# Performance work log

Measured on AMD Instinct MI355X. Metric: run time of the kernel, lower is better.

Reference implementation:

```python
import jax, jax.numpy as jnp
import numpy as np

B, T, C = 2, 2048, 1024
N_HEAD = 16
HEAD_DIM = C // N_HEAD
N_WORLDS = 4


def setup_inputs() -> dict:
    key = jax.random.key(0)
    kx, kq, kk, kv, kp, ka = jax.random.split(key, 6)
    scale = 0.02
    x = jax.random.normal(kx, (B, T, C), dtype=jnp.float32)
    Wq = jax.random.normal(kq, (C, C), dtype=jnp.float32) * scale
    Wk = jax.random.normal(kk, (C, C), dtype=jnp.float32) * scale
    Wv = jax.random.normal(kv, (C, C), dtype=jnp.float32) * scale
    Wproj = jax.random.normal(kp, (C, C), dtype=jnp.float32) * scale
    acc = jax.random.randint(ka, (N_WORLDS, N_WORLDS), 0, 2, dtype=jnp.int32)
    # ensure every world accesses itself so no softmax row is fully masked
    acc = acc.at[jnp.arange(N_WORLDS), jnp.arange(N_WORLDS)].set(1)
    return {"x": x, "Wq": Wq, "Wk": Wk, "Wv": Wv, "Wproj": Wproj,
            "accessibility": acc}


def reference(x, Wq, Wk, Wv, Wproj, accessibility):
    Bd, Td, Cd = x.shape
    # torch Linear: y = x @ W.T  -> project then split heads
    q = (x @ Wq.T).reshape(Bd, Td, N_HEAD, HEAD_DIM).transpose(0, 2, 1, 3)
    k = (x @ Wk.T).reshape(Bd, Td, N_HEAD, HEAD_DIM).transpose(0, 2, 1, 3)
    v = (x @ Wv.T).reshape(Bd, Td, N_HEAD, HEAD_DIM).transpose(0, 2, 1, 3)

    scores = jnp.einsum('bhqd,bhkd->bhqk', q, k) / jnp.sqrt(
        jnp.asarray(HEAD_DIM, dtype=x.dtype))

    # Kripke modal mask: token t lives in world t % n_worlds (necessity: \u25a1)
    world = jnp.arange(Td) % accessibility.shape[0]
    modal_mask = accessibility[world][:, world]          # (T, T) 0/1
    scores = jnp.where(modal_mask[None, None] == 0, -jnp.inf, scores)

    attn = jax.nn.softmax(scores, axis=-1)
    out = jnp.einsum('bhqk,bhkd->bhqd', attn, v)
    out = out.transpose(0, 2, 1, 3).reshape(Bd, Td, Cd)
    return out @ Wproj.T
```

## Files before the change

### kernel.cpp

```cpp
#include <hip/hip_runtime.h>
#include <hip/hip_bf16.h>
#include <stdint.h>


typedef __attribute__((ext_vector_type(8))) __bf16   bf16x8;
typedef __attribute__((ext_vector_type(4))) float    f32x4;
typedef __attribute__((ext_vector_type(8))) ushort   ushort8;

__device__ __forceinline__ ushort f2bf(float x) {
    uint32_t u = __float_as_uint(x);
    return (ushort)((u + 0x7fffu + ((u >> 16) & 1u)) >> 16);
}
__device__ __forceinline__ float sentinel(float v, float s) {
    return (fabsf(v) < 1e30f) ? v : s;
}
__device__ __forceinline__ f32x4 mfma16(bf16x8 a, bf16x8 b, f32x4 c) {
    return __builtin_amdgcn_mfma_f32_16x16x32_bf16(a, b, c, 0, 0, 0);
}
__device__ __forceinline__ ushort2 pk2(float a, float b) {
    __hip_bfloat162 h = __float22bfloat162_rn(make_float2(a, b));
    union { __hip_bfloat162 h; ushort2 u; } c; c.h = h; return c.u;
}
__device__ __forceinline__ ushort4 cvt4(float4 v) {
    ushort2 lo = pk2(v.x, v.y), hi = pk2(v.z, v.w);
    ushort4 r; r.x = lo.x; r.y = lo.y; r.z = hi.x; r.w = hi.y; return r;
}
__device__ __forceinline__ ushort4 cvt4s(float4 v, float s) {
    ushort2 lo = pk2(v.x * s, v.y * s), hi = pk2(v.z * s, v.w * s);
    ushort4 r; r.x = lo.x; r.y = lo.y; r.z = hi.x; r.w = hi.y; return r;
}
__device__ __forceinline__ float fexp2(float x) {
#if __has_builtin(__builtin_amdgcn_exp2f)
    return __builtin_amdgcn_exp2f(x);
#else
    return exp2f(x);
#endif
}
__device__ __forceinline__ void gld16(const ushort* g, ushort* l) {
    auto* g1 = reinterpret_cast<const __attribute__((address_space(1))) uint32_t*>(
        reinterpret_cast<uintptr_t>(g));
    auto* l3 = reinterpret_cast<__attribute__((address_space(3))) uint32_t*>(
        reinterpret_cast<uintptr_t>(l));
    __builtin_amdgcn_global_load_lds(g1, l3, 16, 0, 0);
}

__device__ __forceinline__ int swz(int row, int ch) {
    return row * 64 + ((ch ^ (row & 7)) * 8);
}

#define QSCALE 0.1803368801111244f

__global__ __launch_bounds__(256) void cvt_prepass(
        const float* __restrict__ x,  const float* __restrict__ Wq,
        const float* __restrict__ Wk, const float* __restrict__ Wv,
        const float* __restrict__ Wp,
        ushort* __restrict__ xb,  ushort* __restrict__ wqb,
        ushort* __restrict__ wkb, ushort* __restrict__ wvb,
        ushort* __restrict__ wpb)
{
    int gid = blockIdx.x;
    const float* src; ushort* dst; float sc = 1.0f; int boff;
    if (gid < 4096)      { src = x;  dst = xb;  boff = gid; }
    else if (gid < 5120) { src = Wq; dst = wqb; boff = gid - 4096; sc = QSCALE; }
    else if (gid < 6144) { src = Wk; dst = wkb; boff = gid - 5120; }
    else if (gid < 7168) { src = Wv; dst = wvb; boff = gid - 6144; }
    else                 { src = Wp; dst = wpb; boff = gid - 7168; }
    size_t idx = (size_t)boff * 1024 + threadIdx.x * 4;
    float4 v = *(const float4*)&src[idx];
    *(ushort4*)&dst[idx] = cvt4s(v, sc);
}

__global__ __launch_bounds__(256) void gemm_qkv_b(
        const ushort* __restrict__ xb,
        const ushort* __restrict__ wqb, const ushort* __restrict__ wkb,
        const ushort* __restrict__ wvb,
        ushort* __restrict__ Cq, ushort* __restrict__ Ck,
        ushort* __restrict__ Cv)
{
    __shared__ ushort As[128 * 64];
    __shared__ ushort Bs[128 * 64];

    const int sel = blockIdx.x >> 3;
    const ushort* __restrict__ Bw = sel == 0 ? wqb : (sel == 1 ? wkb : wvb);
    ushort* __restrict__ C        = sel == 0 ? Cq : (sel == 1 ? Ck : Cv);

    const int tid  = threadIdx.x;
    const int lane = tid & 63;
    const int wave = tid >> 6;
    const int quad = lane >> 4;
    const int l15  = lane & 15;
    const int bm = blockIdx.y * 128;
    const int bn = (blockIdx.x & 7) * 128;
    const int wm = (wave & 1) * 64, wn = (wave >> 1) * 64;

    f32x4 acc[4][4] = {};

    for (int k0 = 0; k0 < 1024; k0 += 64) {
        __syncthreads();
        #pragma unroll
        for (int j = 0; j < 4; ++j) {
            int cb = j * 256 + wave * 64;
            int ci = cb + lane;
            int r  = ci >> 3;
            int qc = (ci & 7) ^ (r & 7);
            gld16(&xb[(size_t)(bm + r) * 1024 + k0 + qc * 8], &As[cb * 8]);
            gld16(&Bw[(size_t)(bn + r) * 1024 + k0 + qc * 8], &Bs[cb * 8]);
        }
        __syncthreads();

        bf16x8 af[2][4], bfr[2][4];
        #pragma unroll
        for (int f = 0; f < 2; ++f)
            #pragma unroll
            for (int i = 0; i < 4; ++i) {
                int ch = f * 4 + quad;
                af[f][i]  = *(const bf16x8*)&As[swz(wm + i * 16 + l15, ch)];
                bfr[f][i] = *(const bf16x8*)&Bs[swz(wn + i * 16 + l15, ch)];
            }
        #pragma unroll
        for (int f = 0; f < 2; ++f)
            #pragma unroll
            for (int i = 0; i < 4; ++i)
                #pragma unroll
                for (int t = 0; t < 4; ++t)
                    acc[i][t] = mfma16(af[f][i], bfr[f][t], acc[i][t]);
    }

    if (sel < 2) {
        #pragma unroll
        for (int i = 0; i < 4; ++i)
            #pragma unroll
            for (int t = 0; t < 4; ++t)
                #pragma unroll
                for (int r = 0; r < 4; ++r) {
                    int m = bm + wm + i * 16 + quad * 4 + r;
                    int n = bn + wn + t * 16 + l15;
                    int b = m >> 11, ts = m & 2047, hh = n >> 6, d = n & 63;
                    C[((size_t)((b << 4) | hh) * 2048 + ts) * 64 + d] =
                        f2bf(sentinel(acc[i][t][r], 1e8f));
                }
    } else {
        #pragma unroll
        for (int i = 0; i < 4; ++i)
            #pragma unroll
            for (int t = 0; t < 4; ++t) {
                int m0 = bm + wm + i * 16 + quad * 4;
                int n  = bn + wn + t * 16 + l15;
                int b = m0 >> 11, ts = m0 & 2047, hh = n >> 6, d = n & 63;
                ushort4 hv;
                hv.x = f2bf(sentinel(acc[i][t][0], 1e8f));
                hv.y = f2bf(sentinel(acc[i][t][1], 1e8f));
                hv.z = f2bf(sentinel(acc[i][t][2], 1e8f));
                hv.w = f2bf(sentinel(acc[i][t][3], 1e8f));
                *(ushort4*)&C[((size_t)((b << 4) | hh) * 64 + d) * 2048 + ts] = hv;
            }
    }
}

__global__ __launch_bounds__(256) void gemm_proj_b(
        const ushort* __restrict__ O, const ushort* __restrict__ wpb,
        float* __restrict__ out)
{
    __shared__ ushort As[128 * 64];
    __shared__ ushort Bs[64 * 64];

    const int tid  = threadIdx.x;
    const int lane = tid & 63;
    const int wave = tid >> 6;
    const int quad = lane >> 4;
    const int l15  = lane & 15;
    const int bm = blockIdx.y * 128, bn = blockIdx.x * 64;
    const int wm = (wave & 1) * 64,  wn = (wave >> 1) * 32;

    f32x4 acc[4][2] = {};

    for (int k0 = 0; k0 < 1024; k0 += 64) {
        __syncthreads();
        int h = k0 >> 6;
        #pragma unroll
        for (int j = 0; j < 4; ++j) {
            int cb = j * 256 + wave * 64;
            int ci = cb + lane;
            int r  = ci >> 3;
            int qc = (ci & 7) ^ (r & 7);
            int m = bm + r;
            int b = m >> 11, ts = m & 2047;
            gld16(&O[((((size_t)(b * 16 + h)) * 2048 + ts) << 6) + qc * 8],
                  &As[cb * 8]);
        }
        #pragma unroll
        for (int j = 0; j < 2; ++j) {
            int cb = j * 256 + wave * 64;
            int ci = cb + lane;
            int r  = ci >> 3;
            int qc = (ci & 7) ^ (r & 7);
            gld16(&wpb[(size_t)(bn + r) * 1024 + k0 + qc * 8], &Bs[cb * 8]);
        }
        __syncthreads();

        bf16x8 af[2][4], bfr[2][2];
        #pragma unroll
        for (int f = 0; f < 2; ++f) {
            int ch = f * 4 + quad;
            #pragma unroll
            for (int i = 0; i < 4; ++i)
                af[f][i] = *(const bf16x8*)&As[swz(wm + i * 16 + l15, ch)];
            #pragma unroll
            for (int t = 0; t < 2; ++t)
                bfr[f][t] = *(const bf16x8*)&Bs[swz(wn + t * 16 + l15, ch)];
        }
        #pragma unroll
        for (int f = 0; f < 2; ++f)
            #pragma unroll
            for (int i = 0; i < 4; ++i)
                #pragma unroll
                for (int t = 0; t < 2; ++t)
                    acc[i][t] = mfma16(af[f][i], bfr[f][t], acc[i][t]);
    }

    #pragma unroll
    for (int i = 0; i < 4; ++i)
        #pragma unroll
        for (int t = 0; t < 2; ++t)
            #pragma unroll
            for (int r = 0; r < 4; ++r) {
                int m = bm + wm + i * 16 + quad * 4 + r;
                int n = bn + wn + t * 16 + l15;
                out[(size_t)m * 1024 + n] = sentinel(acc[i][t][r], 100.0f);
            }
}

__global__ __launch_bounds__(256) void attn_kernel(
        ushort* __restrict__ Q, const ushort* __restrict__ Kk,
        const ushort* __restrict__ Vt_g, const int* __restrict__ accm)
{
    __shared__ ushort Ks[2][64 * 64];
    __shared__ ushort Vt[2][64 * 64];
    __shared__ ushort Ps[4][32 * 64];

    const int tid  = threadIdx.x;
    const int lane = tid & 63;
    const int wave = tid >> 6;
    const int quad = lane >> 4;
    const int l15  = lane & 15;
    const int bh = blockIdx.x, qt = blockIdx.y;

    ushort*       Qg = Q    + ((size_t)bh * 2048 + qt * 128) * 64;
    const ushort* Kg = Kk   + (size_t)bh * 2048 * 64;
    const ushort* Vg = Vt_g + (size_t)bh * 64 * 2048;

    bf16x8 aq[2][2];
    #pragma unroll
    for (int i = 0; i < 2; ++i)
        #pragma unroll
        for (int f = 0; f < 2; ++f)
            aq[i][f] = *(const bf16x8*)
                &Qg[(wave * 32 + i * 16 + l15) * 64 + f * 32 + quad * 8];

    f32x4 c0;
    #pragma unroll
    for (int r = 0; r < 4; ++r)
        c0[r] = accm[(l15 & 3) * 4 + r] ? 0.f : -1e30f;

    bf16x8 aones;
    #pragma unroll
    for (int j = 0; j < 8; ++j) aones[j] = (__bf16)1.0f;

    f32x4 oacc[4][2] = {};
    f32x4 lacc[2] = {};

    auto stage = [&](int kt, int buf) {
        #pragma unroll
        for (int j = 0; j < 2; ++j) {
            int cb = j * 256 + wave * 64;
            int ci = cb + lane;
            int r  = ci >> 3;
            int qc = (ci & 7) ^ (r & 7);
            gld16(&Kg[((size_t)kt * 64 + r) * 64 + qc * 8], &Ks[buf][cb * 8]);
            gld16(&Vg[(size_t)r * 2048 + kt * 64 + qc * 8], &Vt[buf][cb * 8]);
        }
    };

    stage(0, 0);
    for (int kt = 0; kt < 32; ++kt) {
        const int cur = kt & 1;
        __syncthreads();
        if (kt < 31) stage(kt + 1, cur ^ 1);

        f32x4 st[4][2];
        #pragma unroll
        for (int k4 = 0; k4 < 4; ++k4) { st[k4][0] = c0; st[k4][1] = c0; }
        #pragma unroll
        for (int f = 0; f < 2; ++f) {
            int ch = f * 4 + quad;
            #pragma unroll
            for (int k4 = 0; k4 < 4; ++k4) {
                bf16x8 ak = *(const bf16x8*)&Ks[cur][swz(k4 * 16 + l15, ch)];
                #pragma unroll
                for (int i = 0; i < 2; ++i)
                    st[k4][i] = mfma16(ak, aq[i][f], st[k4][i]);
            }
        }

        #pragma unroll
        for (int i = 0; i < 2; ++i) {
            int prow = i * 16 + l15;
            #pragma unroll
            for (int k4 = 0; k4 < 4; ++k4) {
                float p0 = fexp2(st[k4][i][0]);
                float p1 = fexp2(st[k4][i][1]);
                float p2 = fexp2(st[k4][i][2]);
                float p3 = fexp2(st[k4][i][3]);
                ushort2 lo = pk2(p0, p1), hi = pk2(p2, p3);
                ushort4 pv4; pv4.x = lo.x; pv4.y = lo.y;
                pv4.z = hi.x; pv4.w = hi.y;
                int pc8 = (k4 * 2 + (quad >> 1)) ^ (l15 & 7);
                *(ushort4*)&Ps[wave][prow * 64 + pc8 * 8 + (quad & 1) * 4] = pv4;
            }
        }

        bf16x8 bp[2][2];
        #pragma unroll
        for (int i = 0; i < 2; ++i)
            #pragma unroll
            for (int f = 0; f < 2; ++f)
                bp[i][f] = *(const bf16x8*)&Ps[wave][swz(i * 16 + l15, f * 4 + quad)];
        #pragma unroll
        for (int f = 0; f < 2; ++f) {
            int ch = f * 4 + quad;
            #pragma unroll
            for (int i = 0; i < 2; ++i)
                lacc[i] = mfma16(aones, bp[i][f], lacc[i]);
            #pragma unroll
            for (int dt = 0; dt < 4; ++dt) {
                bf16x8 av = *(const bf16x8*)&Vt[cur][swz(dt * 16 + l15, ch)];
                #pragma unroll
                for (int i = 0; i < 2; ++i)
                    oacc[dt][i] = mfma16(av, bp[i][f], oacc[dt][i]);
            }
        }
    }

    #pragma unroll
    for (int i = 0; i < 2; ++i) {
        const float inv = 1.0f / lacc[i][0];
        #pragma unroll
        for (int dt = 0; dt < 4; ++dt) {
            ushort4 o4;
            o4.x = f2bf(sentinel(oacc[dt][i][0] * inv, 1e4f));
            o4.y = f2bf(sentinel(oacc[dt][i][1] * inv, 1e4f));
            o4.z = f2bf(sentinel(oacc[dt][i][2] * inv, 1e4f));
            o4.w = f2bf(sentinel(oacc[dt][i][3] * inv, 1e4f));
            *(ushort4*)&Qg[(wave * 32 + i * 16 + l15) * 64 + dt * 16 + quad * 4] = o4;
        }
    }
}

__global__ __launch_bounds__(256) void gemm_qkv_f32(
        const float* __restrict__ A,
        const float* __restrict__ Wq, const float* __restrict__ Wk,
        const float* __restrict__ Wv,
        ushort* __restrict__ Cq, ushort* __restrict__ Ck,
        ushort* __restrict__ Cv)
{
    __shared__ __align__(16) ushort As[128 * 72];
    __shared__ __align__(16) ushort Bs[128 * 72];

    const int sel = blockIdx.x >> 3;
    const float* __restrict__ Bw = sel == 0 ? Wq : (sel == 1 ? Wk : Wv);
    ushort* __restrict__ C       = sel == 0 ? Cq : (sel == 1 ? Ck : Cv);
    const float scale = sel == 0 ? QSCALE : 1.0f;

    const int tid  = threadIdx.x;
    const int lane = tid & 63;
    const int wave = tid >> 6;
    const int quad = lane >> 4;
    const int l15  = lane & 15;
    const int bm = blockIdx.y * 128;
    const int bn = (blockIdx.x & 7) * 128;
    const int wm = (wave & 1) * 64, wn = (wave >> 1) * 64;

    f32x4 acc[4][4] = {};

    for (int k0 = 0; k0 < 1024; k0 += 64) {
        __syncthreads();
        #pragma unroll
        for (int i = 0; i < 8; ++i) {
            int c = tid + 256 * i;
            int row = c >> 4, col = (c & 15) * 4;
            float4 a4 = *(const float4*)&A[(size_t)(bm + row) * 1024 + k0 + col];
            *(ushort4*)&As[row * 72 + col] = cvt4(a4);
            float4 b4 = *(const float4*)&Bw[(size_t)(bn + row) * 1024 + k0 + col];
            *(ushort4*)&Bs[row * 72 + col] = cvt4s(b4, scale);
        }
        __syncthreads();

        bf16x8 af[2][4], bfr[2][4];
        #pragma unroll
        for (int f = 0; f < 2; ++f)
            #pragma unroll
            for (int i = 0; i < 4; ++i) {
                af[f][i]  = *(const bf16x8*)&As[(wm + i * 16 + l15) * 72 + f * 32 + quad * 8];
                bfr[f][i] = *(const bf16x8*)&Bs[(wn + i * 16 + l15) * 72 + f * 32 + quad * 8];
            }
        #pragma unroll
        for (int f = 0; f < 2; ++f)
            #pragma unroll
            for (int i = 0; i < 4; ++i)
                #pragma unroll
                for (int t = 0; t < 4; ++t)
                    acc[i][t] = mfma16(af[f][i], bfr[f][t], acc[i][t]);
    }

    if (sel < 2) {
        #pragma unroll
        for (int i = 0; i < 4; ++i)
            #pragma unroll
            for (int t = 0; t < 4; ++t)
                #pragma unroll
                for (int r = 0; r < 4; ++r) {
                    int m = bm + wm + i * 16 + quad * 4 + r;
                    int n = bn + wn + t * 16 + l15;
                    int b = m >> 11, ts = m & 2047, hh = n >> 6, d = n & 63;
                    C[((size_t)((b << 4) | hh) * 2048 + ts) * 64 + d] =
                        f2bf(sentinel(acc[i][t][r], 1e8f));
                }
    } else {
        #pragma unroll
        for (int i = 0; i < 4; ++i)
            #pragma unroll
            for (int t = 0; t < 4; ++t) {
                int m0 = bm + wm + i * 16 + quad * 4;
                int n  = bn + wn + t * 16 + l15;
                int b = m0 >> 11, ts = m0 & 2047, hh = n >> 6, d = n & 63;
                ushort4 hv;
                hv.x = f2bf(sentinel(acc[i][t][0], 1e8f));
                hv.y = f2bf(sentinel(acc[i][t][1], 1e8f));
                hv.z = f2bf(sentinel(acc[i][t][2], 1e8f));
                hv.w = f2bf(sentinel(acc[i][t][3], 1e8f));
                *(ushort4*)&C[((size_t)((b << 4) | hh) * 64 + d) * 2048 + ts] = hv;
            }
    }
}

__global__ __launch_bounds__(256) void gemm_proj_f32(
        const ushort* __restrict__ A, const float* __restrict__ Bw,
        float* __restrict__ C)
{
    __shared__ __align__(16) ushort As[128 * 72];
    __shared__ __align__(16) ushort Bs[64 * 72];

    const int tid  = threadIdx.x;
    const int lane = tid & 63;
    const int wave = tid >> 6;
    const int quad = lane >> 4;
    const int l15  = lane & 15;
    const int bm = blockIdx.y * 128, bn = blockIdx.x * 64;
    const int wm = (wave & 1) * 64,  wn = (wave >> 1) * 32;

    f32x4 acc[4][2] = {};

    for (int k0 = 0; k0 < 1024; k0 += 64) {
        __syncthreads();
        #pragma unroll
        for (int i = 0; i < 4; ++i) {
            int c = tid + 256 * i;
            int row = c >> 3, col = (c & 7) * 8;
            int m = bm + row;
            int b = m >> 11, ts = m & 2047, h = k0 >> 6;
            size_t aoff = ((((size_t)(b * 16 + h)) * 2048 + ts) << 6) + col;
            *(ushort8*)&As[row * 72 + col] = *(const ushort8*)&A[aoff];
        }
        #pragma unroll
        for (int i = 0; i < 4; ++i) {
            int c = tid + 256 * i;
            int row = c >> 4, col = (c & 15) * 4;
            float4 b4 = *(const float4*)&Bw[(size_t)(bn + row) * 1024 + k0 + col];
            *(ushort4*)&Bs[row * 72 + col] = cvt4(b4);
        }
        __syncthreads();

        bf16x8 af[2][4], bfr[2][2];
        #pragma unroll
        for (int f = 0; f < 2; ++f) {
            #pragma unroll
            for (int i = 0; i < 4; ++i)
                af[f][i] = *(const bf16x8*)&As[(wm + i * 16 + l15) * 72 + f * 32 + quad * 8];
            #pragma unroll
            for (int t = 0; t < 2; ++t)
                bfr[f][t] = *(const bf16x8*)&Bs[(wn + t * 16 + l15) * 72 + f * 32 + quad * 8];
        }
        #pragma unroll
        for (int f = 0; f < 2; ++f)
            #pragma unroll
            for (int i = 0; i < 4; ++i)
                #pragma unroll
                for (int t = 0; t < 2; ++t)
                    acc[i][t] = mfma16(af[f][i], bfr[f][t], acc[i][t]);
    }

    #pragma unroll
    for (int i = 0; i < 4; ++i)
        #pragma unroll
        for (int t = 0; t < 2; ++t)
            #pragma unroll
            for (int r = 0; r < 4; ++r) {
                int m = bm + wm + i * 16 + quad * 4 + r;
                int n = bn + wn + t * 16 + l15;
                C[(size_t)m * 1024 + n] = sentinel(acc[i][t][r], 100.0f);
            }
}

__global__ void diag_kernel(float* out, int n, float val) {
    int i = blockIdx.x * blockDim.x + threadIdx.x;
    if (i < n) out[i] = (i == 0) ? val : 0.f;
}

extern "C" void kernel_launch(void* const* d_in, const int* in_sizes, int n_in,
                              void* d_out, int out_size, void* d_ws, size_t ws_size,
                              hipStream_t stream) {
    const float* x  = (const float*)d_in[0];
    const float* Wq = (const float*)d_in[1];
    const float* Wk = (const float*)d_in[2];
    const float* Wv = (const float*)d_in[3];
    const float* Wp = (const float*)d_in[4];
    const int* accm = (const int*)d_in[5];
    float* out = (float*)d_out;

    const size_t SZ = (size_t)4 * 1024 * 1024;
    const size_t WSZ = (size_t)1024 * 1024;

    if (ws_size < 3 * SZ * sizeof(ushort)) {
        diag_kernel<<<(out_size + 255) / 256, 256, 0, stream>>>(
            out, out_size, (float)ws_size);
        return;
    }

    ushort* k_ws = (ushort*)d_ws;
    ushort* v_ws = k_ws + SZ;
    ushort* q_ws = v_ws + SZ;
    dim3 blk(256);

    const size_t need_fast = (4 * SZ + 4 * WSZ) * sizeof(ushort);
    if (ws_size >= need_fast) {
        ushort* xb  = q_ws + SZ;
        ushort* wqb = xb + SZ;
        ushort* wkb = wqb + WSZ;
        ushort* wvb = wkb + WSZ;
        ushort* wpb = wvb + WSZ;
        cvt_prepass<<<8192, blk, 0, stream>>>(x, Wq, Wk, Wv, Wp,
                                              xb, wqb, wkb, wvb, wpb);
        gemm_qkv_b<<<dim3(24, 32), blk, 0, stream>>>(xb, wqb, wkb, wvb,
                                                     q_ws, k_ws, v_ws);
        attn_kernel<<<dim3(32, 16), blk, 0, stream>>>(q_ws, k_ws, v_ws, accm);
        gemm_proj_b<<<dim3(16, 32), blk, 0, stream>>>(q_ws, wpb, out);
    } else {
        gemm_qkv_f32<<<dim3(24, 32), blk, 0, stream>>>(x, Wq, Wk, Wv,
                                                       q_ws, k_ws, v_ws);
        attn_kernel<<<dim3(32, 16), blk, 0, stream>>>(q_ws, k_ws, v_ws, accm);
        gemm_proj_f32<<<dim3(16, 32), blk, 0, stream>>>(q_ws, Wp, out);
    }
}
```

Measured before the change: 190.7 us.

## Group tokens by world and skip inaccessible key tiles in attention

The QKV GEMM epilogues now write Q, K and V in a world-permuted token order, so that each block of 512 consecutive positions holds one world's tokens. The attention kernel reads the accessibility row for its query world and iterates only over the key tiles belonging to accessible worlds, dropping the additive mask init. The projection GEMM reads O through the same permutation. This removes the masked-out QK and PV work, but V stores become scalar strided writes instead of a packed ushort4 store, and it relies on T being a multiple of four times the world count.

```diff
diff --git a/kernel.cpp b/kernel.cpp
--- a/kernel.cpp
+++ b/kernel.cpp
@@ -46,6 +46,10 @@
 
 __device__ __forceinline__ int swz(int row, int ch) {
     return row * 64 + ((ch ^ (row & 7)) * 8);
+}
+
+__device__ __forceinline__ int wperm(int ts) {
+    return ((ts & 3) << 9) | (ts >> 2);
 }
 
 #define QSCALE 0.1803368801111244f
@@ -136,7 +140,7 @@
                     int m = bm + wm + i * 16 + quad * 4 + r;
                     int n = bn + wn + t * 16 + l15;
                     int b = m >> 11, ts = m & 2047, hh = n >> 6, d = n & 63;
-                    C[((size_t)((b << 4) | hh) * 2048 + ts) * 64 + d] =
+                    C[((size_t)((b << 4) | hh) * 2048 + wperm(ts)) * 64 + d] =
                         f2bf(sentinel(acc[i][t][r], 1e8f));
                 }
     } else {
@@ -146,13 +150,12 @@
             for (int t = 0; t < 4; ++t) {
                 int m0 = bm + wm + i * 16 + quad * 4;
                 int n  = bn + wn + t * 16 + l15;
-                int b = m0 >> 11, ts = m0 & 2047, hh = n >> 6, d = n & 63;
-                ushort4 hv;
-                hv.x = f2bf(sentinel(acc[i][t][0], 1e8f));
-                hv.y = f2bf(sentinel(acc[i][t][1], 1e8f));
-                hv.z = f2bf(sentinel(acc[i][t][2], 1e8f));
-                hv.w = f2bf(sentinel(acc[i][t][3], 1e8f));
-                *(ushort4*)&C[((size_t)((b << 4) | hh) * 64 + d) * 2048 + ts] = hv;
+                int b = m0 >> 11, ts0 = m0 & 2047, hh = n >> 6, d = n & 63;
+                size_t base = ((size_t)((b << 4) | hh) * 64 + d) * 2048
+                            + (ts0 >> 2);
+                #pragma unroll
+                for (int r = 0; r < 4; ++r)
+                    C[base + (r << 9)] = f2bf(sentinel(acc[i][t][r], 1e8f));
             }
     }
 }
@@ -185,7 +188,7 @@
             int qc = (ci & 7) ^ (r & 7);
             int m = bm + r;
             int b = m >> 11, ts = m & 2047;
-            gld16(&O[((((size_t)(b * 16 + h)) * 2048 + ts) << 6) + qc * 8],
+            gld16(&O[((((size_t)(b * 16 + h)) * 2048 + wperm(ts)) << 6) + qc * 8],
                   &As[cb * 8]);
         }
         #pragma unroll
@@ -249,6 +252,16 @@
     const ushort* Kg = Kk   + (size_t)bh * 2048 * 64;
     const ushort* Vg = Vt_g + (size_t)bh * 64 * 2048;
 
+    const int qworld = qt >> 2;
+    int gpack = 0, ng = 0;
+    #pragma unroll
+    for (int w = 0; w < 4; ++w)
+        if (accm[qworld * 4 + w] != 0) { gpack |= w << (ng * 8); ++ng; }
+    const int nkt = ng * 8;
+    auto ktof = [&](int i) {
+        return ((((gpack >> ((i >> 3) << 3)) & 3) << 3) | (i & 7));
+    };
+
     bf16x8 aq[2][2];
     #pragma unroll
     for (int i = 0; i < 2; ++i)
@@ -256,11 +269,6 @@
         for (int f = 0; f < 2; ++f)
             aq[i][f] = *(const bf16x8*)
                 &Qg[(wave * 32 + i * 16 + l15) * 64 + f * 32 + quad * 8];
-
-    f32x4 c0;
-    #pragma unroll
-    for (int r = 0; r < 4; ++r)
-        c0[r] = accm[(l15 & 3) * 4 + r] ? 0.f : -1e30f;
 
     bf16x8 aones;
     #pragma unroll
@@ -281,15 +289,13 @@
         }
     };
 
-    stage(0, 0);
-    for (int kt = 0; kt < 32; ++kt) {
-        const int cur = kt & 1;
-        __syncthreads();
-        if (kt < 31) stage(kt + 1, cur ^ 1);
-
-        f32x4 st[4][2];
-        #pragma unroll
-        for (int k4 = 0; k4 < 4; ++k4) { st[k4][0] = c0; st[k4][1] = c0; }
+    stage(ktof(0), 0);
+    for (int it = 0; it < nkt; ++it) {
+        const int cur = it & 1;
+        __syncthreads();
+        if (it < nkt - 1) stage(ktof(it + 1), cur ^ 1);
+
+        f32x4 st[4][2] = {};
         #pragma unroll
         for (int f = 0; f < 2; ++f) {
             int ch = f * 4 + quad;
@@ -422,7 +428,7 @@
                     int m = bm + wm + i * 16 + quad * 4 + r;
                     int n = bn + wn + t * 16 + l15;
                     int b = m >> 11, ts = m & 2047, hh = n >> 6, d = n & 63;
-                    C[((size_t)((b << 4) | hh) * 2048 + ts) * 64 + d] =
+                    C[((size_t)((b << 4) | hh) * 2048 + wperm(ts)) * 64 + d] =
                         f2bf(sentinel(acc[i][t][r], 1e8f));
                 }
     } else {
@@ -432,13 +438,12 @@
             for (int t = 0; t < 4; ++t) {
                 int m0 = bm + wm + i * 16 + quad * 4;
                 int n  = bn + wn + t * 16 + l15;
-                int b = m0 >> 11, ts = m0 & 2047, hh = n >> 6, d = n & 63;
-                ushort4 hv;
-                hv.x = f2bf(sentinel(acc[i][t][0], 1e8f));
-                hv.y = f2bf(sentinel(acc[i][t][1], 1e8f));
-                hv.z = f2bf(sentinel(acc[i][t][2], 1e8f));
-                hv.w = f2bf(sentinel(acc[i][t][3], 1e8f));
-                *(ushort4*)&C[((size_t)((b << 4) | hh) * 64 + d) * 2048 + ts] = hv;
+                int b = m0 >> 11, ts0 = m0 & 2047, hh = n >> 6, d = n & 63;
+                size_t base = ((size_t)((b << 4) | hh) * 64 + d) * 2048
+                            + (ts0 >> 2);
+                #pragma unroll
+                for (int r = 0; r < 4; ++r)
+                    C[base + (r << 9)] = f2bf(sentinel(acc[i][t][r], 1e8f));
             }
     }
 }
@@ -468,7 +473,7 @@
             int row = c >> 3, col = (c & 7) * 8;
             int m = bm + row;
             int b = m >> 11, ts = m & 2047, h = k0 >> 6;
-            size_t aoff = ((((size_t)(b * 16 + h)) * 2048 + ts) << 6) + col;
+            size_t aoff = ((((size_t)(b * 16 + h)) * 2048 + wperm(ts)) << 6) + col;
             *(ushort8*)&As[row * 72 + col] = *(const ushort8*)&A[aoff];
         }
         #pragma unroll
```

Result: faster. 182.1 us (-4.5%).
